# Kernel optimization log

Hardware: AMD Instinct MI355X
Metric: run time of the kernel (lower is better)

## Reference

```python
import jax, jax.numpy as jnp
import numpy as np

B, H, W, C = 4, 64, 64, 32
M1 = M2 = 16
N = H * W          # 4096 grid nodes per sample
E = 131072         # edges (avg degree 32)
EDIM = 6           # edge feature dim
KMID = 64          # kernel MLP hidden width
EPS = 1e-5         # InstanceNorm eps


def _gelu(x):
    return jax.nn.gelu(x, approximate=False)  # torch nn.GELU default is exact erf


def _mlp(x, w1, b1, w2, b2):
    return _gelu(x @ w1 + b1) @ w2 + b2


def _inorm(x):
    # torch InstanceNorm2d(affine=False) applied to [B,H,W,C]: normalizes over last two dims
    m = x.mean(axis=(2, 3), keepdims=True)
    v = x.var(axis=(2, 3), keepdims=True)
    return (x - m) * jax.lax.rsqrt(v + EPS)


def _lin_init(k, fin, fout):
    lim = 1.0 / np.sqrt(fin)
    kw, kb = jax.random.split(k)
    w = jax.random.uniform(kw, (fin, fout), jnp.float32, -lim, lim)
    b = jax.random.uniform(kb, (fout,), jnp.float32, -lim, lim)
    return w, b


def setup_inputs() -> dict:
    key = jax.random.key(0)
    ks = jax.random.split(key, 14)
    s = 1.0 / (C * C)
    inp = {}
    inp['nodes'] = jax.random.normal(ks[0], (B, H, W, C), jnp.float32)
    inp['edge_index'] = jax.random.randint(ks[1], (2, E), 0, N, dtype=jnp.int64)
    inp['edge_attr'] = jax.random.uniform(ks[2], (E, EDIM), jnp.float32)
    # spectral conv complex weights, stored as real/imag float32 pairs
    inp['w1_re'] = s * jax.random.uniform(ks[3], (C, C, M1, M2), jnp.float32)
    inp['w1_im'] = s * jax.random.uniform(ks[4], (C, C, M1, M2), jnp.float32)
    inp['w2_re'] = s * jax.random.uniform(ks[5], (C, C, M1, M2), jnp.float32)
    inp['w2_im'] = s * jax.random.uniform(ks[6], (C, C, M1, M2), jnp.float32)
    # self.mlp : MLP(C, C, 2C)
    inp['mlp_w1'], inp['mlp_b1'] = _lin_init(ks[7], C, 2 * C)
    inp['mlp_w2'], inp['mlp_b2'] = _lin_init(ks[8], 2 * C, C)
    # self.w : MLP(C, C, 2C)
    inp['wm_w1'], inp['wm_b1'] = _lin_init(ks[9], C, 2 * C)
    inp['wm_w2'], inp['wm_b2'] = _lin_init(ks[10], 2 * C, C)
    # GNO kernel MLP : EDIM -> KMID -> C*C
    inp['ker_w1'], inp['ker_b1'] = _lin_init(ks[11], EDIM, KMID)
    inp['ker_w2'], inp['ker_b2'] = _lin_init(ks[12], KMID, C * C)
    # NNConv root weight and bias (PyG uniform(size) init with size=in_channels)
    lim = 1.0 / np.sqrt(C)
    kr, kb = jax.random.split(ks[13])
    inp['root'] = jax.random.uniform(kr, (C, C), jnp.float32, -lim, lim)
    inp['gbias'] = jax.random.uniform(kb, (C,), jnp.float32, -lim, lim)
    return inp


def reference(nodes, edge_index, edge_attr, w1_re, w1_im, w2_re, w2_im,
              mlp_w1, mlp_b1, mlp_w2, mlp_b2, wm_w1, wm_b1, wm_w2, wm_b2,
              ker_w1, ker_b1, ker_w2, ker_b2, root, gbias):
    x = _inorm(nodes)                                             # [B,H,W,C]

    # --- spectral conv branch ---
    x_ft = jnp.fft.rfftn(x, axes=(1, 2), norm='ortho')            # [B,H,W//2+1,C]
    w1 = (w1_re + 1j * w1_im).astype(jnp.complex64)
    w2 = (w2_re + 1j * w2_im).astype(jnp.complex64)
    top = jnp.einsum('bxyi,ioxy->bxyo', x_ft[:, :M1, :M2, :], w1)
    bot = jnp.einsum('bxyi,ioxy->bxyo', x_ft[:, -M1:, :M2, :], w2)
    out_ft = jnp.zeros((B, H, W // 2 + 1, C), jnp.complex64)
    out_ft = out_ft.at[:, :M1, :M2, :].set(top).at[:, -M1:, :M2, :].set(bot)
    x1 = jnp.fft.irfftn(out_ft, axes=(1, 2), s=(H, W), norm='ortho')
    x1 = _mlp(_inorm(x1), mlp_w1, mlp_b1, mlp_w2, mlp_b2)         # [B,H,W,C]

    # --- pointwise MLP branch ---
    x2 = _inorm(_mlp(x, wm_w1, wm_b1, wm_w2, wm_b2))              # [B,H,W,C]

    # --- edge-conditioned GNO branch ---
    x3 = x.reshape(B, N, C)
    wmat = _mlp(edge_attr, ker_w1, ker_b1, ker_w2, ker_b2).reshape(E, C, C)
    src, dst = edge_index[0], edge_index[1]
    msg = jnp.einsum('bec,eco->beo', x3[:, src, :], wmat)         # [B,E,C]
    agg = jnp.zeros((B, N, C), jnp.float32).at[:, dst, :].add(msg)
    x3 = agg + x3 @ root + gbias                                  # [B,N,C]

    return _gelu(x1 + x2 + x3.reshape(B, H, W, C))
```

## Files before the change

### kernel.cpp

```cpp
#include <hip/hip_runtime.h>

#define E_ 131072

typedef _Float16 half8 __attribute__((ext_vector_type(8)));
typedef float f32x4 __attribute__((ext_vector_type(4)));

__device__ __forceinline__ float gelu_f(float x) {
    return 0.5f * x * (1.0f + erff(x * 0.70710678118654752f));
}

#define TWOPI_64 (6.2831853071795864769f / 64.0f)

__device__ __forceinline__ void block_reduce2(float& s, float& s2, float* red) {
    #pragma unroll
    for (int off = 32; off > 0; off >>= 1) {
        s  += __shfl_down(s, off, 64);
        s2 += __shfl_down(s2, off, 64);
    }
    int lane = threadIdx.x & 63, wv = threadIdx.x >> 6;
    __syncthreads();
    if (lane == 0) { red[wv] = s; red[wv + 4] = s2; }
    __syncthreads();
    s  = red[0] + red[1] + red[2] + red[3];
    s2 = red[4] + red[5] + red[6] + red[7];
}

__device__ __forceinline__ void gno_body(int e0, float* sbufF, float* sB2, int* ssrc, int* sdst,
                                         const float* __restrict__ ea,
                                         const float* __restrict__ kw1, const float* __restrict__ kb1,
                                         const float* __restrict__ kb2,
                                         const _Float16* __restrict__ whi,
                                         const float* __restrict__ xn, const int* __restrict__ ei,
                                         float* __restrict__ agg) {
    _Float16* sxTh = (_Float16*)sbufF;
    int t = threadIdx.x;
    int lane = t & 63, wv = t >> 6, quad = lane >> 4, l15 = lane & 15;
    int eg = wv >> 1, t2 = wv & 1;

    if (t < 64) ssrc[t] = ei[e0 + t];
    else if (t < 128) sdst[t - 64] = ei[E_ + e0 + t - 64];
    for (int f = t; f < 1024; f += 256) sB2[f] = kb2[f];
    {
        int r = t >> 2, k0 = (t & 3) * 16;
        const float* ep = ea + (e0 + r) * 6;
        float e6[6];
        #pragma unroll
        for (int d = 0; d < 6; ++d) e6[d] = ep[d];
        #pragma unroll
        for (int kk = 0; kk < 16; ++kk) {
            int k = k0 + kk;
            float acc = kb1[k];
            #pragma unroll
            for (int d = 0; d < 6; ++d) acc += e6[d] * kw1[d * 64 + k];
            sbufF[r * 68 + k] = gelu_f(acc);
        }
    }
    __syncthreads();
    half8 ahi[2][2], alo[2][2];
    #pragma unroll
    for (int et = 0; et < 2; ++et) {
        #pragma unroll
        for (int kh = 0; kh < 2; ++kh) {
            const float* hp = sbufF + (eg * 32 + et * 16 + l15) * 68 + kh * 32 + quad * 8;
            float4 h0 = *(const float4*)hp;
            float4 h1 = *(const float4*)(hp + 4);
            float hv[8] = {h0.x, h0.y, h0.z, h0.w, h1.x, h1.y, h1.z, h1.w};
            half8 hh, hl;
            #pragma unroll
            for (int j = 0; j < 8; ++j) {
                _Float16 hi = (_Float16)hv[j];
                hh[j] = hi;
                hl[j] = (_Float16)(hv[j] - (float)hi);
            }
            ahi[et][kh] = hh;
            alo[et][kh] = hl;
        }
    }
    __syncthreads();
    {
        int b = t & 3, r = t >> 2;
        int s = ssrc[r];
        int pe = (r >> 5) * 32 + ((r >> 2) & 3) * 8 + ((r >> 4) & 1) * 4 + (r & 3);
        const float4* xp = (const float4*)(xn + (b * 4096 + s) * 32);
        _Float16* dp = sxTh + b * 2312 + pe;
        #pragma unroll
        for (int q = 0; q < 8; ++q) {
            float4 v = xp[q];
            dp[(q * 4 + 0) * 72] = (_Float16)v.x;
            dp[(q * 4 + 1) * 72] = (_Float16)v.y;
            dp[(q * 4 + 2) * 72] = (_Float16)v.z;
            dp[(q * 4 + 3) * 72] = (_Float16)v.w;
        }
    }
    __syncthreads();
    float msg[4][2][4];
    #pragma unroll
    for (int b = 0; b < 4; ++b)
        #pragma unroll
        for (int et = 0; et < 2; ++et)
            #pragma unroll
            for (int r = 0; r < 4; ++r) msg[b][et][r] = 0.f;

    for (int i = 0; i < 32; ++i) {
        float b2v = sB2[i * 32 + t2 * 16 + l15];
        int f0 = (i * 4 + t2 * 2) * 512 + lane * 8;
        half8 bhi0 = *(const half8*)(whi + f0);
        half8 bhi1 = *(const half8*)(whi + f0 + 512);
        f32x4 acc[2];
        #pragma unroll
        for (int et = 0; et < 2; ++et) {
            f32x4 ac = {b2v, b2v, b2v, b2v};
            ac = __builtin_amdgcn_mfma_f32_16x16x32_f16(ahi[et][0], bhi0, ac, 0, 0, 0);
            ac = __builtin_amdgcn_mfma_f32_16x16x32_f16(ahi[et][1], bhi1, ac, 0, 0, 0);
            ac = __builtin_amdgcn_mfma_f32_16x16x32_f16(alo[et][0], bhi0, ac, 0, 0, 0);
            ac = __builtin_amdgcn_mfma_f32_16x16x32_f16(alo[et][1], bhi1, ac, 0, 0, 0);
            acc[et] = ac;
        }
        #pragma unroll
        for (int b = 0; b < 4; ++b) {
            const half8 xv = *(const half8*)(sxTh + b * 2312 + i * 72 + eg * 32 + quad * 8);
            #pragma unroll
            for (int et = 0; et < 2; ++et) {
                msg[b][et][0] += (float)xv[et * 4 + 0] * acc[et][0];
                msg[b][et][1] += (float)xv[et * 4 + 1] * acc[et][1];
                msg[b][et][2] += (float)xv[et * 4 + 2] * acc[et][2];
                msg[b][et][3] += (float)xv[et * 4 + 3] * acc[et][3];
            }
        }
    }
    int o = t2 * 16 + l15;
    #pragma unroll
    for (int et = 0; et < 2; ++et) {
        #pragma unroll
        for (int r = 0; r < 4; ++r) {
            int row = eg * 32 + et * 16 + quad * 4 + r;
            int d = sdst[row];
            #pragma unroll
            for (int b = 0; b < 4; ++b) {
                atomicAdd(&agg[(b * 4096 + d) * 32 + o], msg[b][et][r]);
            }
        }
    }
}

__global__ __launch_bounds__(256, 4) void k_pre(const float* __restrict__ nodes,
                                                const float* __restrict__ w2,
                                                float* __restrict__ xn,
                                                float* __restrict__ agg,
                                                float* __restrict__ Gre, float* __restrict__ Gim,
                                                _Float16* __restrict__ whi) {
    int t = threadIdx.x;
    if (blockIdx.x >= 256) {
        int g0 = (blockIdx.x - 256) * 512 + t;
        #pragma unroll 1
        for (int rep = 0; rep < 2; ++rep) {
            int g = g0 + rep * 256;
            int j = g & 7, l = (g >> 3) & 63, fid = g >> 9;
            int i = fid >> 2, t2 = (fid >> 1) & 1, kh = fid & 1;
            int quad = l >> 4, l15 = l & 15;
            int k = kh * 32 + quad * 8 + j;
            int n = i * 32 + t2 * 16 + l15;
            whi[g] = (_Float16)w2[k * 1024 + n];
        }
        return;
    }
    int bh = blockIdx.x;
    __shared__ float sx[2048];
    __shared__ float tc[64], ts[64];
    __shared__ float red[8];
    const float4* src = (const float4*)(nodes + bh * 2048);
    float4* dst = (float4*)(xn + bh * 2048);
    float4* az = (float4*)(agg + bh * 2048);
    if (t < 64) { float a = TWOPI_64 * t; tc[t] = cosf(a); ts[t] = sinf(a); }
    float4 v0 = src[t * 2], v1 = src[t * 2 + 1];
    float s  = v0.x + v0.y + v0.z + v0.w + v1.x + v1.y + v1.z + v1.w;
    float s2 = v0.x*v0.x + v0.y*v0.y + v0.z*v0.z + v0.w*v0.w
             + v1.x*v1.x + v1.y*v1.y + v1.z*v1.z + v1.w*v1.w;
    block_reduce2(s, s2, red);
    float mean = s * (1.0f / 2048.0f);
    float var  = s2 * (1.0f / 2048.0f) - mean * mean;
    float sc = rsqrtf(var + 1e-5f);
    v0.x = (v0.x - mean) * sc; v0.y = (v0.y - mean) * sc;
    v0.z = (v0.z - mean) * sc; v0.w = (v0.w - mean) * sc;
    v1.x = (v1.x - mean) * sc; v1.y = (v1.y - mean) * sc;
    v1.z = (v1.z - mean) * sc; v1.w = (v1.w - mean) * sc;
    dst[t * 2] = v0; dst[t * 2 + 1] = v1;
    float4 z = {0.f, 0.f, 0.f, 0.f};
    az[t * 2] = z; az[t * 2 + 1] = z;
    ((float4*)sx)[t * 2] = v0;
    ((float4*)sx)[t * 2 + 1] = v1;
    __syncthreads();
    #pragma unroll 1
    for (int rep = 0; rep < 2; ++rep) {
        int oi = rep * 256 + t;
        int ky = oi >> 5, i = oi & 31;
        float re = 0.f, im = 0.f;
        #pragma unroll 8
        for (int w = 0; w < 64; ++w) {
            float v = sx[w * 32 + i];
            int m = (ky * w) & 63;
            re += v * tc[m];
            im -= v * ts[m];
        }
        Gre[bh * 512 + oi] = re;
        Gim[bh * 512 + oi] = im;
    }
}

__global__ __launch_bounds__(256, 4) void k_g1(
        const float* __restrict__ Gre, const float* __restrict__ Gim,
        const float* __restrict__ w1re, const float* __restrict__ w1im,
        const float* __restrict__ w2re, const float* __restrict__ w2im,
        float* __restrict__ Yr, float* __restrict__ Yi,
        const float* __restrict__ ww1, const float* __restrict__ wb1,
        const float* __restrict__ ww2, const float* __restrict__ wb2,
        float* __restrict__ osum,
        const float* __restrict__ ea,
        const float* __restrict__ kw1, const float* __restrict__ kb1,
        const float* __restrict__ kb2,
        const _Float16* __restrict__ whi,
        const float* __restrict__ xn,
        const int* __restrict__ ei,
        float* __restrict__ agg) {
    __shared__ __align__(16) float U[5648];
    __shared__ int ssrc[64], sdst[64];
    int t = threadIdx.x;

    if (blockIdx.x < 128) {
        float* tc  = U;
        float* ts  = U + 64;
        float* sXr = U + 128;
        float* sXi = U + 656;
        int bid = blockIdx.x;
        int b = bid >> 5, kxi = bid & 31;
        int kx = kxi + (kxi < 16 ? 0 : 32);
        int x = kxi & 15;
        const float* wre = (kxi < 16) ? w1re : w2re;
        const float* wim = (kxi < 16) ? w1im : w2im;
        if (t < 64) { float a = TWOPI_64 * t; tc[t] = cosf(a); ts[t] = sinf(a); }
        __syncthreads();
        #pragma unroll 1
        for (int rep = 0; rep < 2; ++rep) {
            int oi = rep * 256 + t;
            int ky = oi >> 5, i = oi & 31;
            float re = 0.f, im = 0.f;
            #pragma unroll 8
            for (int h = 0; h < 64; ++h) {
                int gidx = (b * 64 + h) * 512 + ky * 32 + i;
                float gr = Gre[gidx], gi = Gim[gidx];
                int m = (kx * h) & 63;
                float c = tc[m], sv = ts[m];
                re += gr * c + gi * sv;
                im += gi * c - gr * sv;
            }
            sXr[ky * 33 + i] = re;
            sXi[ky * 33 + i] = im;
        }
        __syncthreads();
        #pragma unroll 1
        for (int rep = 0; rep < 2; ++rep) {
            int oi = rep * 256 + t;
            int ky = oi & 15, o = oi >> 4;
            float re = 0.f, im = 0.f;
            #pragma unroll 4
            for (int i = 0; i < 32; ++i) {
                float xr = sXr[ky * 33 + i], xi = sXi[ky * 33 + i];
                int widx = (i * 32 + o) * 256 + x * 16 + ky;
                float wr = wre[widx], wi = wim[widx];
                re += xr * wr - xi * wi;
                im += xr * wi + xi * wr;
            }
            Yr[bid * 512 + ky * 32 + o] = re;
            Yi[bid * 512 + ky * 32 + o] = im;
        }
        return;
    }
    if (blockIdx.x < 384) {
        int bh = blockIdx.x - 128;
        float* red = U;
        float* sX = U + 8;
        _Float16* sHh = (_Float16*)(U + 2120);
        for (int f = t; f < 2048; f += 256) sX[(f >> 5) * 33 + (f & 31)] = xn[bh * 2048 + f];
        __syncthreads();
        #pragma unroll 1
        for (int rep = 0; rep < 16; ++rep) {
            int idx = rep * 256 + t;
            int w = idx >> 6, k = idx & 63;
            float acc = wb1[k];
            #pragma unroll 4
            for (int c = 0; c < 32; ++c) acc += sX[w * 33 + c] * ww1[c * 64 + k];
            sHh[w * 72 + k] = (_Float16)gelu_f(acc);
        }
        __syncthreads();
        float s = 0.f, s2 = 0.f;
        #pragma unroll 1
        for (int rep = 0; rep < 8; ++rep) {
            int idx = rep * 256 + t;
            int w = idx >> 5, o = idx & 31;
            float acc = wb2[o];
            #pragma unroll 4
            for (int k = 0; k < 64; ++k) acc += (float)sHh[w * 72 + k] * ww2[k * 32 + o];
            sX[w * 33 + o] = acc;
            s += acc; s2 += acc * acc;
        }
        block_reduce2(s, s2, red);
        float mean = s * (1.0f / 2048.0f);
        float sc = rsqrtf(s2 * (1.0f / 2048.0f) - mean * mean + 1e-5f);
        #pragma unroll 1
        for (int rep = 0; rep < 8; ++rep) {
            int idx = rep * 256 + t;
            int w = idx >> 5, o = idx & 31;
            osum[bh * 2048 + idx] = (sX[w * 33 + o] - mean) * sc;
        }
        return;
    }
    gno_body((blockIdx.x - 384) * 64, U, U + 4624, ssrc, sdst,
             ea, kw1, kb1, kb2, whi, xn, ei, agg);
}

__global__ __launch_bounds__(256, 4) void k_g2(
        const float* __restrict__ Yr, const float* __restrict__ Yi,
        const float* __restrict__ mw1, const float* __restrict__ mb1,
        const float* __restrict__ mw2, const float* __restrict__ mb2,
        float* __restrict__ osum,
        const float* __restrict__ ea,
        const float* __restrict__ kw1, const float* __restrict__ kb1,
        const float* __restrict__ kb2,
        const _Float16* __restrict__ whi,
        const float* __restrict__ xn,
        const int* __restrict__ ei,
        float* __restrict__ agg) {
    __shared__ __align__(16) float U[5648];
    __shared__ int ssrc[64], sdst[64];
    int t = threadIdx.x;

    if (blockIdx.x < 256) {
        int bh = blockIdx.x;
        int b = bh >> 6, h = bh & 63;
        float* tc  = U;
        float* ts  = U + 64;
        float* red = U + 128;
        float* sZr = U + 136;
        float* sZi = U + 664;
        float* sP  = U + 1192;
        _Float16* sHh = (_Float16*)(U + 3304);
        if (t < 64) { float a = TWOPI_64 * t; tc[t] = cosf(a); ts[t] = sinf(a); }
        __syncthreads();
        #pragma unroll 1
        for (int rep = 0; rep < 2; ++rep) {
            int oi = rep * 256 + t;
            int ky = oi >> 5, o = oi & 31;
            float re = 0.f, im = 0.f;
            #pragma unroll 4
            for (int kxi = 0; kxi < 32; ++kxi) {
                int kx = kxi + (kxi < 16 ? 0 : 32);
                int m = (kx * h) & 63;
                float c = tc[m], sv = ts[m];
                int yidx = (b * 32 + kxi) * 512 + ky * 32 + o;
                float yr = Yr[yidx], yi = Yi[yidx];
                re += yr * c - yi * sv;
                im += yr * sv + yi * c;
            }
            sZr[ky * 33 + o] = re;
            sZi[ky * 33 + o] = im;
        }
        __syncthreads();
        float s = 0.f, s2 = 0.f;
        #pragma unroll 1
        for (int rep = 0; rep < 8; ++rep) {
            int idx = rep * 256 + t;
            int w = idx >> 5, o = idx & 31;
            float acc = sZr[o];
            #pragma unroll
            for (int ky = 1; ky < 16; ++ky) {
                int m = (ky * w) & 63;
                acc += 2.0f * (sZr[ky * 33 + o] * tc[m] - sZi[ky * 33 + o] * ts[m]);
            }
            acc *= (1.0f / 4096.0f);
            sP[w * 33 + o] = acc;
            s += acc; s2 += acc * acc;
        }
        block_reduce2(s, s2, red);
        float mean = s * (1.0f / 2048.0f);
        float sc = rsqrtf(s2 * (1.0f / 2048.0f) - mean * mean + 1e-5f);
        #pragma unroll 1
        for (int rep = 0; rep < 8; ++rep) {
            int idx = rep * 256 + t;
            int w = idx >> 5, o = idx & 31;
            sP[w * 33 + o] = (sP[w * 33 + o] - mean) * sc;
        }
        __syncthreads();
        #pragma unroll 1
        for (int rep = 0; rep < 16; ++rep) {
            int idx = rep * 256 + t;
            int w = idx >> 6, k = idx & 63;
            float acc = mb1[k];
            #pragma unroll 4
            for (int c = 0; c < 32; ++c) acc += sP[w * 33 + c] * mw1[c * 64 + k];
            sHh[w * 72 + k] = (_Float16)gelu_f(acc);
        }
        __syncthreads();
        #pragma unroll 1
        for (int rep = 0; rep < 8; ++rep) {
            int idx = rep * 256 + t;
            int w = idx >> 5, o = idx & 31;
            float acc = mb2[o];
            #pragma unroll 4
            for (int k = 0; k < 64; ++k) acc += (float)sHh[w * 72 + k] * mw2[k * 32 + o];
            osum[bh * 2048 + idx] += acc;
        }
        return;
    }
    gno_body((1024 + blockIdx.x - 256) * 64, U, U + 4624, ssrc, sdst,
             ea, kw1, kb1, kb2, whi, xn, ei, agg);
}

__global__ __launch_bounds__(256, 4) void k_final(const float* __restrict__ osum, const float* __restrict__ agg,
                                                  const float* __restrict__ xn, const float* __restrict__ root,
                                                  const float* __restrict__ gbias, float* __restrict__ out) {
    int bh = blockIdx.x >> 2, q = blockIdx.x & 3;
    int base = bh * 2048 + q * 512;
    int t = threadIdx.x;
    __shared__ float sX[16 * 33];
    __shared__ float sR[1024];
    for (int f = t; f < 512; f += 256) sX[(f >> 5) * 33 + (f & 31)] = xn[base + f];
    for (int f = t; f < 1024; f += 256) sR[f] = root[f];
    __syncthreads();
    #pragma unroll 1
    for (int rep = 0; rep < 2; ++rep) {
        int idx = rep * 256 + t;
        int w = idx >> 5, o = idx & 31;
        float acc = gbias[o] + osum[base + idx] + agg[base + idx];
        #pragma unroll 4
        for (int c = 0; c < 32; ++c) acc += sX[w * 33 + c] * sR[c * 32 + o];
        out[base + idx] = gelu_f(acc);
    }
}

extern "C" void kernel_launch(void* const* d_in, const int* in_sizes, int n_in,
                              void* d_out, int out_size, void* d_ws, size_t ws_size,
                              hipStream_t stream) {
    (void)in_sizes; (void)n_in; (void)out_size; (void)ws_size;
    const float* nodes  = (const float*)d_in[0];
    const int*   eidx   = (const int*)d_in[1];
    const float* eattr  = (const float*)d_in[2];
    const float* w1re   = (const float*)d_in[3];
    const float* w1im   = (const float*)d_in[4];
    const float* w2re   = (const float*)d_in[5];
    const float* w2im   = (const float*)d_in[6];
    const float* mlp_w1 = (const float*)d_in[7];
    const float* mlp_b1 = (const float*)d_in[8];
    const float* mlp_w2 = (const float*)d_in[9];
    const float* mlp_b2 = (const float*)d_in[10];
    const float* wm_w1  = (const float*)d_in[11];
    const float* wm_b1  = (const float*)d_in[12];
    const float* wm_w2  = (const float*)d_in[13];
    const float* wm_b2  = (const float*)d_in[14];
    const float* ker_w1 = (const float*)d_in[15];
    const float* ker_b1 = (const float*)d_in[16];
    const float* ker_w2 = (const float*)d_in[17];
    const float* ker_b2 = (const float*)d_in[18];
    const float* root   = (const float*)d_in[19];
    const float* gbias  = (const float*)d_in[20];
    float* out = (float*)d_out;

    char* ws = (char*)d_ws;
    size_t off = 0;
    auto alloc = [&](size_t bytes) {
        void* p = ws + off;
        off += (bytes + 255) & ~(size_t)255;
        return p;
    };
    float* xn   = (float*)alloc(524288 * 4);
    float* agg  = (float*)alloc(524288 * 4);
    float* osum = (float*)alloc(524288 * 4);
    float* Gre  = (float*)alloc(131072 * 4);
    float* Gim  = (float*)alloc(131072 * 4);
    float* Yr   = (float*)alloc(65536 * 4);
    float* Yi   = (float*)alloc(65536 * 4);
    _Float16* whi = (_Float16*)alloc(65536 * 2);

    k_pre<<<384, 256, 0, stream>>>(nodes, ker_w2, xn, agg, Gre, Gim, whi);
    k_g1<<<1408, 256, 0, stream>>>(Gre, Gim, w1re, w1im, w2re, w2im, Yr, Yi,
                                   wm_w1, wm_b1, wm_w2, wm_b2, osum,
                                   eattr, ker_w1, ker_b1, ker_b2, whi, xn, eidx, agg);
    k_g2<<<1280, 256, 0, stream>>>(Yr, Yi, mlp_w1, mlp_b1, mlp_w2, mlp_b2, osum,
                                   eattr, ker_w1, ker_b1, ker_b2, whi, xn, eidx, agg);
    k_final<<<1024, 256, 0, stream>>>(osum, agg, xn, root, gbias, out);
}
```

Before: 238.4 us.

## Counting-sort edges by destination and merge consecutive same-destination atomics

```diff
diff --git a/kernel.cpp b/kernel.cpp
--- a/kernel.cpp
+++ b/kernel.cpp
@@ -26,23 +26,24 @@
 }
 
 __device__ __forceinline__ void gno_body(int e0, float* sbufF, float* sB2, int* ssrc, int* sdst,
-                                         const float* __restrict__ ea,
+                                         const float* __restrict__ easrt,
                                          const float* __restrict__ kw1, const float* __restrict__ kb1,
                                          const float* __restrict__ kb2,
                                          const _Float16* __restrict__ whi,
-                                         const float* __restrict__ xn, const int* __restrict__ ei,
+                                         const float* __restrict__ xn,
+                                         const int* __restrict__ srcs, const int* __restrict__ dsts,
                                          float* __restrict__ agg) {
     _Float16* sxTh = (_Float16*)sbufF;
     int t = threadIdx.x;
     int lane = t & 63, wv = t >> 6, quad = lane >> 4, l15 = lane & 15;
     int eg = wv >> 1, t2 = wv & 1;
 
-    if (t < 64) ssrc[t] = ei[e0 + t];
-    else if (t < 128) sdst[t - 64] = ei[E_ + e0 + t - 64];
+    if (t < 64) ssrc[t] = srcs[e0 + t];
+    else if (t < 128) sdst[t - 64] = dsts[e0 + t - 64];
     for (int f = t; f < 1024; f += 256) sB2[f] = kb2[f];
     {
         int r = t >> 2, k0 = (t & 3) * 16;
-        const float* ep = ea + (e0 + r) * 6;
+        const float* ep = easrt + (e0 + r) * 6;
         float e6[6];
         #pragma unroll
         for (int d = 0; d < 6; ++d) e6[d] = ep[d];
@@ -131,14 +132,20 @@
     int o = t2 * 16 + l15;
     #pragma unroll
     for (int et = 0; et < 2; ++et) {
-        #pragma unroll
-        for (int r = 0; r < 4; ++r) {
-            int row = eg * 32 + et * 16 + quad * 4 + r;
-            int d = sdst[row];
-            #pragma unroll
-            for (int b = 0; b < 4; ++b) {
-                atomicAdd(&agg[(b * 4096 + d) * 32 + o], msg[b][et][r]);
-            }
+        int rowb = eg * 32 + et * 16 + quad * 4;
+        int d0 = sdst[rowb], d1 = sdst[rowb + 1], d2 = sdst[rowb + 2], d3 = sdst[rowb + 3];
+        bool f0 = (d0 != d1), f1 = (d1 != d2), f2 = (d2 != d3);
+        #pragma unroll
+        for (int b = 0; b < 4; ++b) {
+            float* ag = agg + b * 131072 + o;
+            float s = msg[b][et][0];
+            if (f0) { atomicAdd(ag + d0 * 32, s); s = 0.f; }
+            s += msg[b][et][1];
+            if (f1) { atomicAdd(ag + d1 * 32, s); s = 0.f; }
+            s += msg[b][et][2];
+            if (f2) { atomicAdd(ag + d2 * 32, s); s = 0.f; }
+            s += msg[b][et][3];
+            atomicAdd(ag + d3 * 32, s);
         }
     }
 }
@@ -148,8 +155,14 @@
                                                 float* __restrict__ xn,
                                                 float* __restrict__ agg,
                                                 float* __restrict__ Gre, float* __restrict__ Gim,
-                                                _Float16* __restrict__ whi) {
+                                                _Float16* __restrict__ whi,
+                                                int* __restrict__ hist) {
     int t = threadIdx.x;
+    if (blockIdx.x >= 384) {
+        #pragma unroll
+        for (int j = 0; j < 16; ++j) hist[j * 256 + t] = 0;
+        return;
+    }
     if (blockIdx.x >= 256) {
         int g0 = (blockIdx.x - 256) * 512 + t;
         #pragma unroll 1
@@ -207,6 +220,61 @@
     }
 }
 
+__global__ __launch_bounds__(256, 4) void k_hist(const int* __restrict__ ei, int* __restrict__ hist) {
+    int e0 = blockIdx.x * 2048 + threadIdx.x;
+    #pragma unroll
+    for (int r = 0; r < 8; ++r) atomicAdd(&hist[ei[E_ + e0 + r * 256]], 1);
+}
+
+__global__ __launch_bounds__(256, 4) void k_scan(const int* __restrict__ hist, int* __restrict__ cursor) {
+    __shared__ int sh[4096];
+    __shared__ int wsum[4];
+    int t = threadIdx.x;
+    for (int i = t; i < 4096; i += 256) sh[i] = hist[i];
+    __syncthreads();
+    int p = 0;
+    #pragma unroll
+    for (int j = 0; j < 16; ++j) p += sh[t * 16 + j];
+    int lane = t & 63, wv = t >> 6;
+    int v = p;
+    #pragma unroll
+    for (int off = 1; off < 64; off <<= 1) {
+        int u = __shfl_up(v, off, 64);
+        if (lane >= off) v += u;
+    }
+    if (lane == 63) wsum[wv] = v;
+    __syncthreads();
+    int wo = 0;
+    for (int w = 0; w < wv; ++w) wo += wsum[w];
+    int run = wo + v - p;
+    #pragma unroll
+    for (int j = 0; j < 16; ++j) {
+        int b = t * 16 + j;
+        int h = sh[b];
+        cursor[b] = run;
+        run += h;
+    }
+}
+
+__global__ __launch_bounds__(256, 4) void k_scatter(const int* __restrict__ ei, const float* __restrict__ ea,
+                                                    int* __restrict__ cursor,
+                                                    int* __restrict__ srcsrt, int* __restrict__ dstsrt,
+                                                    float* __restrict__ easrt) {
+    int e0 = blockIdx.x * 2048 + threadIdx.x;
+    #pragma unroll 1
+    for (int r = 0; r < 8; ++r) {
+        int e = e0 + r * 256;
+        int d = ei[E_ + e];
+        int pos = atomicAdd(&cursor[d], 1);
+        srcsrt[pos] = ei[e];
+        dstsrt[pos] = d;
+        const float* sp = ea + e * 6;
+        float* dp = easrt + pos * 6;
+        #pragma unroll
+        for (int j = 0; j < 6; ++j) dp[j] = sp[j];
+    }
+}
+
 __global__ __launch_bounds__(256, 4) void k_g1(
         const float* __restrict__ Gre, const float* __restrict__ Gim,
         const float* __restrict__ w1re, const float* __restrict__ w1im,
@@ -215,12 +283,12 @@
         const float* __restrict__ ww1, const float* __restrict__ wb1,
         const float* __restrict__ ww2, const float* __restrict__ wb2,
         float* __restrict__ osum,
-        const float* __restrict__ ea,
+        const float* __restrict__ easrt,
         const float* __restrict__ kw1, const float* __restrict__ kb1,
         const float* __restrict__ kb2,
         const _Float16* __restrict__ whi,
         const float* __restrict__ xn,
-        const int* __restrict__ ei,
+        const int* __restrict__ srcsrt, const int* __restrict__ dstsrt,
         float* __restrict__ agg) {
     __shared__ __align__(16) float U[5648];
     __shared__ int ssrc[64], sdst[64];
@@ -315,7 +383,7 @@
         return;
     }
     gno_body((blockIdx.x - 384) * 64, U, U + 4624, ssrc, sdst,
-             ea, kw1, kb1, kb2, whi, xn, ei, agg);
+             easrt, kw1, kb1, kb2, whi, xn, srcsrt, dstsrt, agg);
 }
 
 __global__ __launch_bounds__(256, 4) void k_g2(
@@ -323,12 +391,12 @@
         const float* __restrict__ mw1, const float* __restrict__ mb1,
         const float* __restrict__ mw2, const float* __restrict__ mb2,
         float* __restrict__ osum,
-        const float* __restrict__ ea,
+        const float* __restrict__ easrt,
         const float* __restrict__ kw1, const float* __restrict__ kb1,
         const float* __restrict__ kb2,
         const _Float16* __restrict__ whi,
         const float* __restrict__ xn,
-        const int* __restrict__ ei,
+        const int* __restrict__ srcsrt, const int* __restrict__ dstsrt,
         float* __restrict__ agg) {
     __shared__ __align__(16) float U[5648];
     __shared__ int ssrc[64], sdst[64];
@@ -412,7 +480,7 @@
         return;
     }
     gno_body((1024 + blockIdx.x - 256) * 64, U, U + 4624, ssrc, sdst,
-             ea, kw1, kb1, kb2, whi, xn, ei, agg);
+             easrt, kw1, kb1, kb2, whi, xn, srcsrt, dstsrt, agg);
 }
 
 __global__ __launch_bounds__(256, 4) void k_final(const float* __restrict__ osum, const float* __restrict__ agg,
@@ -479,12 +547,20 @@
     float* Yr   = (float*)alloc(65536 * 4);
     float* Yi   = (float*)alloc(65536 * 4);
     _Float16* whi = (_Float16*)alloc(65536 * 2);
-
-    k_pre<<<384, 256, 0, stream>>>(nodes, ker_w2, xn, agg, Gre, Gim, whi);
+    int*   hist   = (int*)alloc(4096 * 4);
+    int*   cursor = (int*)alloc(4096 * 4);
+    int*   srcsrt = (int*)alloc(131072 * 4);
+    int*   dstsrt = (int*)alloc(131072 * 4);
+    float* easrt  = (float*)alloc(131072 * 6 * 4);
+
+    k_pre<<<385, 256, 0, stream>>>(nodes, ker_w2, xn, agg, Gre, Gim, whi, hist);
+    k_hist<<<64, 256, 0, stream>>>(eidx, hist);
+    k_scan<<<1, 256, 0, stream>>>(hist, cursor);
+    k_scatter<<<64, 256, 0, stream>>>(eidx, eattr, cursor, srcsrt, dstsrt, easrt);
     k_g1<<<1408, 256, 0, stream>>>(Gre, Gim, w1re, w1im, w2re, w2im, Yr, Yi,
                                    wm_w1, wm_b1, wm_w2, wm_b2, osum,
-                                   eattr, ker_w1, ker_b1, ker_b2, whi, xn, eidx, agg);
+                                   easrt, ker_w1, ker_b1, ker_b2, whi, xn, srcsrt, dstsrt, agg);
     k_g2<<<1280, 256, 0, stream>>>(Yr, Yi, mlp_w1, mlp_b1, mlp_w2, mlp_b2, osum,
-                                   eattr, ker_w1, ker_b1, ker_b2, whi, xn, eidx, agg);
+                                   easrt, ker_w1, ker_b1, ker_b2, whi, xn, srcsrt, dstsrt, agg);
     k_final<<<1024, 256, 0, stream>>>(osum, agg, xn, root, gbias, out);
 }
```

Result: slower. 265.6 us (+11.4%).

## Schedule GNO edge chunks via a global atomic work queue

Applied to the files above, without the earlier changes.

```diff
diff --git a/kernel.cpp b/kernel.cpp
--- a/kernel.cpp
+++ b/kernel.cpp
@@ -148,8 +148,10 @@
                                                 float* __restrict__ xn,
                                                 float* __restrict__ agg,
                                                 float* __restrict__ Gre, float* __restrict__ Gim,
-                                                _Float16* __restrict__ whi) {
+                                                _Float16* __restrict__ whi,
+                                                int* __restrict__ qctr) {
     int t = threadIdx.x;
+    if (blockIdx.x == 0 && t < 2) qctr[t] = 0;
     if (blockIdx.x >= 256) {
         int g0 = (blockIdx.x - 256) * 512 + t;
         #pragma unroll 1
@@ -221,9 +223,11 @@
         const _Float16* __restrict__ whi,
         const float* __restrict__ xn,
         const int* __restrict__ ei,
-        float* __restrict__ agg) {
+        float* __restrict__ agg,
+        int* __restrict__ qctr) {
     __shared__ __align__(16) float U[5648];
     __shared__ int ssrc[64], sdst[64];
+    __shared__ int sChunk;
     int t = threadIdx.x;
 
     if (blockIdx.x < 128) {
@@ -273,9 +277,7 @@
             Yr[bid * 512 + ky * 32 + o] = re;
             Yi[bid * 512 + ky * 32 + o] = im;
         }
-        return;
-    }
-    if (blockIdx.x < 384) {
+    } else if (blockIdx.x < 384) {
         int bh = blockIdx.x - 128;
         float* red = U;
         float* sX = U + 8;
@@ -312,10 +314,16 @@
             int w = idx >> 5, o = idx & 31;
             osum[bh * 2048 + idx] = (sX[w * 33 + o] - mean) * sc;
         }
-        return;
-    }
-    gno_body((blockIdx.x - 384) * 64, U, U + 4624, ssrc, sdst,
-             ea, kw1, kb1, kb2, whi, xn, ei, agg);
+    }
+    for (;;) {
+        if (t == 0) sChunk = atomicAdd(&qctr[0], 1);
+        __syncthreads();
+        int c = sChunk;
+        if (c >= 1024) break;
+        gno_body(c * 64, U, U + 4624, ssrc, sdst,
+                 ea, kw1, kb1, kb2, whi, xn, ei, agg);
+        __syncthreads();
+    }
 }
 
 __global__ __launch_bounds__(256, 4) void k_g2(
@@ -329,9 +337,11 @@
         const _Float16* __restrict__ whi,
         const float* __restrict__ xn,
         const int* __restrict__ ei,
-        float* __restrict__ agg) {
+        float* __restrict__ agg,
+        int* __restrict__ qctr) {
     __shared__ __align__(16) float U[5648];
     __shared__ int ssrc[64], sdst[64];
+    __shared__ int sChunk;
     int t = threadIdx.x;
 
     if (blockIdx.x < 256) {
@@ -409,10 +419,16 @@
             for (int k = 0; k < 64; ++k) acc += (float)sHh[w * 72 + k] * mw2[k * 32 + o];
             osum[bh * 2048 + idx] += acc;
         }
-        return;
-    }
-    gno_body((1024 + blockIdx.x - 256) * 64, U, U + 4624, ssrc, sdst,
-             ea, kw1, kb1, kb2, whi, xn, ei, agg);
+    }
+    for (;;) {
+        if (t == 0) sChunk = atomicAdd(&qctr[1], 1);
+        __syncthreads();
+        int c = sChunk;
+        if (c >= 1024) break;
+        gno_body((1024 + c) * 64, U, U + 4624, ssrc, sdst,
+                 ea, kw1, kb1, kb2, whi, xn, ei, agg);
+        __syncthreads();
+    }
 }
 
 __global__ __launch_bounds__(256, 4) void k_final(const float* __restrict__ osum, const float* __restrict__ agg,
@@ -479,12 +495,13 @@
     float* Yr   = (float*)alloc(65536 * 4);
     float* Yi   = (float*)alloc(65536 * 4);
     _Float16* whi = (_Float16*)alloc(65536 * 2);
-
-    k_pre<<<384, 256, 0, stream>>>(nodes, ker_w2, xn, agg, Gre, Gim, whi);
-    k_g1<<<1408, 256, 0, stream>>>(Gre, Gim, w1re, w1im, w2re, w2im, Yr, Yi,
+    int* qctr = (int*)alloc(256);
+
+    k_pre<<<384, 256, 0, stream>>>(nodes, ker_w2, xn, agg, Gre, Gim, whi, qctr);
+    k_g1<<<1664, 256, 0, stream>>>(Gre, Gim, w1re, w1im, w2re, w2im, Yr, Yi,
                                    wm_w1, wm_b1, wm_w2, wm_b2, osum,
-                                   eattr, ker_w1, ker_b1, ker_b2, whi, xn, eidx, agg);
-    k_g2<<<1280, 256, 0, stream>>>(Yr, Yi, mlp_w1, mlp_b1, mlp_w2, mlp_b2, osum,
-                                   eattr, ker_w1, ker_b1, ker_b2, whi, xn, eidx, agg);
+                                   eattr, ker_w1, ker_b1, ker_b2, whi, xn, eidx, agg, qctr);
+    k_g2<<<1536, 256, 0, stream>>>(Yr, Yi, mlp_w1, mlp_b1, mlp_w2, mlp_b2, osum,
+                                   eattr, ker_w1, ker_b1, ker_b2, whi, xn, eidx, agg, qctr);
     k_final<<<1024, 256, 0, stream>>>(osum, agg, xn, root, gbias, out);
 }
```

New measurement: 264.1 us. 10.8% more time.
